# Kernel optimization log

Measured on AMD Instinct MI355X. Metric: run time of the kernel, lower is better.

Reference implementation:

```python
import jax, jax.numpy as jnp
import numpy as np

DIM = 128
HEADS = 4
GH, GW = 14, 14
N = GH * GW            # 196
POS_DIM = (DIM // 4) // 4  # 8, per DynamicPosBias(dim//4): pos_dim = (dim//4)//4
B_ = 1024
NW = 64
EPS = 1e-5


def _make_bias_tables():
    # biases: all relative (dh, dw) offsets, shape ((2*GH-1)*(2*GW-1), 2)
    h = np.arange(1 - GH, GH)
    w = np.arange(1 - GW, GW)
    bh, bw = np.meshgrid(h, w, indexing='ij')
    biases = np.stack([bh.ravel(), bw.ravel()], axis=1).astype(np.float32)
    # relative_position_index: (N, N) int
    ch, cw = np.meshgrid(np.arange(GH), np.arange(GW), indexing='ij')
    coords = np.stack([ch.ravel(), cw.ravel()])          # (2, N)
    rel = coords[:, :, None] - coords[:, None, :]        # (2, N, N)
    rel = rel.transpose(1, 2, 0).copy()
    rel[:, :, 0] += GH - 1
    rel[:, :, 1] += GW - 1
    rel[:, :, 0] *= 2 * GW - 1
    idx = rel.sum(-1).astype(np.int32)                   # (N, N)
    return jnp.asarray(biases), jnp.asarray(idx)


def setup_inputs() -> dict:
    key = jax.random.key(0)
    ks = jax.random.split(key, 12)
    s_in = 1.0 / np.sqrt(DIM)
    s_p = 1.0 / np.sqrt(POS_DIM)
    biases, rel_idx = _make_bias_tables()
    return {
        'x': jax.random.normal(ks[0], (B_, N, DIM), jnp.float32),
        'mask': jnp.zeros((NW, N, N), jnp.float32),
        # qkv / proj (stored as (in, out), i.e. torch weight transposed)
        'qkv_w': jax.random.normal(ks[1], (DIM, 3 * DIM), jnp.float32) * s_in,
        'qkv_b': jnp.zeros((3 * DIM,), jnp.float32),
        'proj_w': jax.random.normal(ks[2], (DIM, DIM), jnp.float32) * s_in,
        'proj_b': jnp.zeros((DIM,), jnp.float32),
        # DynamicPosBias params
        'pos_proj_w': jax.random.normal(ks[3], (2, POS_DIM), jnp.float32) * 0.5,
        'pos_proj_b': jnp.zeros((POS_DIM,), jnp.float32),
        'ln1_w': jnp.ones((POS_DIM,), jnp.float32), 'ln1_b': jnp.zeros((POS_DIM,), jnp.float32),
        'fc1_w': jax.random.normal(ks[4], (POS_DIM, POS_DIM), jnp.float32) * s_p,
        'fc1_b': jnp.zeros((POS_DIM,), jnp.float32),
        'ln2_w': jnp.ones((POS_DIM,), jnp.float32), 'ln2_b': jnp.zeros((POS_DIM,), jnp.float32),
        'fc2_w': jax.random.normal(ks[5], (POS_DIM, POS_DIM), jnp.float32) * s_p,
        'fc2_b': jnp.zeros((POS_DIM,), jnp.float32),
        'ln3_w': jnp.ones((POS_DIM,), jnp.float32), 'ln3_b': jnp.zeros((POS_DIM,), jnp.float32),
        'fc3_w': jax.random.normal(ks[6], (POS_DIM, HEADS), jnp.float32) * s_p,
        'fc3_b': jnp.zeros((HEADS,), jnp.float32),
        'biases': biases,       # ((2GH-1)*(2GW-1), 2) float32
        'rel_idx': rel_idx,     # (N, N) int32
    }


def _ln(x, w, b):
    mu = x.mean(-1, keepdims=True)
    var = ((x - mu) ** 2).mean(-1, keepdims=True)
    return (x - mu) * jax.lax.rsqrt(var + EPS) * w + b


def reference(x, mask, qkv_w, qkv_b, proj_w, proj_b,
              pos_proj_w, pos_proj_b,
              ln1_w, ln1_b, fc1_w, fc1_b,
              ln2_w, ln2_b, fc2_w, fc2_b,
              ln3_w, ln3_b, fc3_w, fc3_b,
              biases, rel_idx):
    B, n, C = x.shape
    hd = C // HEADS
    scale = hd ** -0.5

    qkv = (x @ qkv_w + qkv_b).reshape(B, n, 3, HEADS, hd)
    q, k, v = jnp.moveaxis(qkv, 2, 0)          # each (B, n, H, hd)
    q = q * scale
    attn = jnp.einsum('bqhd,bkhd->bhqk', q, k)  # (B, H, n, n)

    # DynamicPosBias (residual=False): pos3(pos2(pos1(pos_proj(biases))))
    p = biases @ pos_proj_w + pos_proj_b
    p = jax.nn.relu(_ln(p, ln1_w, ln1_b)) @ fc1_w + fc1_b
    p = jax.nn.relu(_ln(p, ln2_w, ln2_b)) @ fc2_w + fc2_b
    p = jax.nn.relu(_ln(p, ln3_w, ln3_b)) @ fc3_w + fc3_b   # (L, H)
    rpb = p[rel_idx]                            # (n, n, H) gather
    attn = attn + jnp.transpose(rpb, (2, 0, 1))[None]

    nW = mask.shape[0]
    attn = attn.reshape(B // nW, nW, HEADS, n, n) + mask[None, :, None]
    attn = jax.nn.softmax(attn.reshape(B, HEADS, n, n), axis=-1)

    out = jnp.einsum('bhqk,bkhd->bqhd', attn, v).reshape(B, n, C)
    return out @ proj_w + proj_b
```

## Files before the change

kernel.cpp:

```cpp
#include <hip/hip_runtime.h>
#include <stdint.h>

#define N_TOK 196
#define DIM   128
#define HEADS 4
#define NWIN  64
#define SCALE 0.17677669529663687f
#define PS_LD 232

typedef __bf16 bf16x8 __attribute__((ext_vector_type(8)));
typedef float  f32x4  __attribute__((ext_vector_type(4)));

__device__ __forceinline__ unsigned short f2bf(float f) {
  unsigned r;
  asm("v_cvt_pk_bf16_f32 %0, %1, %2" : "=v"(r) : "v"(f), "v"(f));
  return (unsigned short)r;
}
__device__ __forceinline__ unsigned pack2(float a, float b) {
  unsigned r;
  asm("v_cvt_pk_bf16_f32 %0, %1, %2" : "=v"(r) : "v"(a), "v"(b));
  return r;
}

__global__ void prep_kernel(
    const float* __restrict__ qkv_w, const float* __restrict__ proj_w,
    const float* __restrict__ biases,
    const float* __restrict__ pos_proj_w, const float* __restrict__ pos_proj_b,
    const float* __restrict__ ln1_w, const float* __restrict__ ln1_b,
    const float* __restrict__ fc1_w, const float* __restrict__ fc1_b,
    const float* __restrict__ ln2_w, const float* __restrict__ ln2_b,
    const float* __restrict__ fc2_w, const float* __restrict__ fc2_b,
    const float* __restrict__ ln3_w, const float* __restrict__ ln3_b,
    const float* __restrict__ fc3_w, const float* __restrict__ fc3_b,
    unsigned short* __restrict__ wqkv_t, unsigned short* __restrict__ wproj_t,
    float* __restrict__ ptab)
{
  const int tid = threadIdx.x, blk = blockIdx.x;
  if (blk < 3) {
    int r = blk * 256 + tid;
    if (r < 729) {
      float v[8], t[8];
      float b0 = biases[2*r], b1 = biases[2*r+1];
      for (int j = 0; j < 8; ++j)
        v[j] = b0 * pos_proj_w[j] + b1 * pos_proj_w[8+j] + pos_proj_b[j];
      const float* lws[3] = {ln1_w, ln2_w, ln3_w};
      const float* lbs[3] = {ln1_b, ln2_b, ln3_b};
      const float* fws[3] = {fc1_w, fc2_w, fc3_w};
      const float* fbs[3] = {fc1_b, fc2_b, fc3_b};
      for (int L = 0; L < 3; ++L) {
        float mu = 0.f;  for (int j=0;j<8;++j) mu += v[j];  mu *= 0.125f;
        float var = 0.f; for (int j=0;j<8;++j){ float d=v[j]-mu; var+=d*d; } var *= 0.125f;
        float rs = rsqrtf(var + 1e-5f);
        for (int j=0;j<8;++j){ float u=(v[j]-mu)*rs*lws[L][j]+lbs[L][j]; t[j]=fmaxf(u,0.f); }
        int nout = (L==2) ? 4 : 8;
        for (int o=0;o<nout;++o){ float s=fbs[L][o]; for (int j=0;j<8;++j) s += t[j]*fws[L][j*nout+o]; v[o]=s; }
      }
      for (int hh=0; hh<4; ++hh) ptab[r*4+hh] = v[hh];
    }
  } else if (blk < 7) {
    for (int i = (blk-3)*256 + tid; i < 384*128; i += 1024) {
      int col = i >> 7, k = i & 127;
      wqkv_t[i] = f2bf(qkv_w[k*384 + col]);
    }
  } else {
    for (int i = tid; i < 128*128; i += 256) {
      int col = i >> 7, k = i & 127;
      wproj_t[i] = f2bf(proj_w[k*128 + col]);
    }
  }
}

__global__ void comb_kernel(const int* __restrict__ rel_idx,
                            const float* __restrict__ ptab,
                            const float* __restrict__ mask,
                            float* __restrict__ combT)
{
  int blk = blockIdx.x;
  int w = blk / 196, k = blk - w*196;
  int q = threadIdx.x;
  if (q < N_TOK) {
    int idx = rel_idx[q*N_TOK + k];
    float mv = mask[((size_t)w*N_TOK + q)*N_TOK + k];
    #pragma unroll
    for (int h = 0; h < 4; ++h)
      combT[((size_t)(w*4 + h)*196 + k)*196 + q] = ptab[idx*4 + h] + mv;
  }
}

__launch_bounds__(256, 2)
__global__ void qkv_kernel(const float* __restrict__ x,
                           const float* __restrict__ qkv_b,
                           const unsigned short* __restrict__ wqkv_t,
                           unsigned short* __restrict__ q_g,
                           unsigned short* __restrict__ k_g,
                           unsigned short* __restrict__ vt_g)
{
  const int tid = threadIdx.x;
  const int wave = tid >> 6, lane = tid & 63, lr = lane & 15, lg = lane >> 4;
  const int b = blockIdx.x;
  const float* xb = x + (size_t)b * (N_TOK*DIM);

  bf16x8 wf[6][4];
  float  bq[6];
  f32x4  bv[6];
  #pragma unroll
  for (int i = 0; i < 6; ++i) {
    const int g = wave*6 + i;
    #pragma unroll
    for (int kc = 0; kc < 4; ++kc)
      wf[i][kc] = *(const bf16x8*)(wqkv_t + (g*16 + lr)*128 + kc*32 + lg*8);
    if (g < 16) {
      bq[i] = qkv_b[g*16 + lr];
      bv[i] = (f32x4){0.f,0.f,0.f,0.f};
    } else {
      bq[i] = 0.f;
      #pragma unroll
      for (int r = 0; r < 4; ++r) bv[i][r] = qkv_b[g*16 + lg*4 + r];
    }
  }

  auto load_xf = [&](int rt, bf16x8* xf) {
    const int arow = rt*16 + lr;
    #pragma unroll
    for (int kc = 0; kc < 4; ++kc) {
      union { unsigned u[4]; bf16x8 v; } c;
      if (arow < N_TOK) {
        float4 p0 = *(const float4*)(xb + arow*DIM + kc*32 + lg*8);
        float4 p1 = *(const float4*)(xb + arow*DIM + kc*32 + lg*8 + 4);
        c.u[0] = pack2(p0.x, p0.y); c.u[1] = pack2(p0.z, p0.w);
        c.u[2] = pack2(p1.x, p1.y); c.u[3] = pack2(p1.z, p1.w);
      } else {
        c.u[0] = c.u[1] = c.u[2] = c.u[3] = 0u;
      }
      xf[kc] = c.v;
    }
  };

  bf16x8 xf[4], xfn[4];
  load_xf(0, xf);
  for (int rt = 0; rt < 13; ++rt) {
    if (rt < 12) load_xf(rt + 1, xfn);
    #pragma unroll
    for (int i = 0; i < 6; ++i) {
      const int g = wave*6 + i;
      f32x4 acc = {0.f,0.f,0.f,0.f};
      if (g >= 16) {
        #pragma unroll
        for (int kc = 0; kc < 4; ++kc)
          acc = __builtin_amdgcn_mfma_f32_16x16x32_bf16(wf[i][kc], xf[kc], acc, 0, 0, 0);
        const int dt = g - 16;
        #pragma unroll
        for (int r = 0; r < 4; ++r)
          vt_g[((size_t)b*128 + dt*16 + lg*4 + r)*224 + rt*16 + lr] =
              f2bf(acc[r] + bv[i][r]);
      } else {
        #pragma unroll
        for (int kc = 0; kc < 4; ++kc)
          acc = __builtin_amdgcn_mfma_f32_16x16x32_bf16(xf[kc], wf[i][kc], acc, 0, 0, 0);
        const int cs = (g < 8) ? g*16 : (g-8)*16;
        unsigned short* dst = (g < 8) ? q_g : k_g;
        const float mul = (g < 8) ? SCALE : 1.f;
        #pragma unroll
        for (int r = 0; r < 4; ++r)
          dst[((size_t)(b*4 + (cs>>5))*208 + rt*16 + lg*4 + r)*32 + (cs&31) + lr] =
              f2bf((acc[r] + bq[i]) * mul);
      }
    }
    #pragma unroll
    for (int kc = 0; kc < 4; ++kc) xf[kc] = xfn[kc];
  }
}

__launch_bounds__(256, 3)
__global__ void attn_kernel(const unsigned short* __restrict__ q_g,
                            const unsigned short* __restrict__ k_g,
                            const unsigned short* __restrict__ vt_g,
                            const float* __restrict__ combT,
                            float* __restrict__ out)
{
  __shared__ unsigned short psw_all[4*16*PS_LD];
  const int tid = threadIdx.x;
  const int wave = tid >> 6, lane = tid & 63, lr = lane & 15, lg = lane >> 4;
  const int wgt = blockIdx.x;
  const int v  = (wgt & 7)*512 + (wgt >> 3);
  const int bi = v & 15, wh = v >> 4;
  const int b  = bi*64 + (wh >> 2), h = wh & 3;
  const int bh = b*4 + h;
  unsigned short* psw = psw_all + wave*(16*PS_LD);

  for (int i = lane; i < 256; i += 64)
    psw[(i >> 4)*PS_LD + 208 + (i & 15)] = 0;

  const unsigned short* qb = q_g + (size_t)bh*(208*32);
  const unsigned short* kb = k_g + (size_t)bh*(208*32);
  const unsigned short* vb = vt_g + (size_t)bh*(32*224);
  const float* cbase = combT + (size_t)wh*(196*196);

  bf16x8 kfr[13];
  #pragma unroll
  for (int kt = 0; kt < 13; ++kt)
    kfr[kt] = *(const bf16x8*)(kb + (kt*16 + lr)*32 + lg*8);

  for (int qt = wave; qt < 13; qt += 4) {
    bf16x8 aq = *(const bf16x8*)(qb + (qt*16 + lr)*32 + lg*8);

    f32x4 s[13];
    #pragma unroll
    for (int kt = 0; kt < 13; ++kt) {
      int c = kt*16 + lr;
      s[kt] = (c < N_TOK) ? *(const f32x4*)(cbase + (size_t)c*196 + qt*16 + lg*4)
                          : (f32x4){0.f,0.f,0.f,0.f};
    }

    __builtin_amdgcn_s_setprio(1);
    #pragma unroll
    for (int kt = 0; kt < 13; ++kt)
      s[kt] = __builtin_amdgcn_mfma_f32_16x16x32_bf16(aq, kfr[kt], s[kt], 0, 0, 0);
    __builtin_amdgcn_s_setprio(0);

    #pragma unroll
    for (int kt = 0; kt < 13; ++kt) {
      #pragma unroll
      for (int r = 0; r < 4; ++r) s[kt][r] = __expf(s[kt][r]);
    }
    if (lr >= 4) s[12] = (f32x4){0.f,0.f,0.f,0.f};

    float linv[4];
    #pragma unroll
    for (int r = 0; r < 4; ++r) {
      float ssum = 0.f;
      #pragma unroll
      for (int kt = 0; kt < 13; ++kt) ssum += s[kt][r];
      #pragma unroll
      for (int off = 1; off < 16; off <<= 1) ssum += __shfl_xor(ssum, off);
      linv[r] = 1.f / ssum;
    }

    #pragma unroll
    for (int r = 0; r < 4; ++r) {
      int prow = lg*4 + r;
      #pragma unroll
      for (int kt = 0; kt < 13; ++kt)
        psw[prow*PS_LD + kt*16 + lr] = f2bf(s[kt][r]);
    }
    asm volatile("s_waitcnt lgkmcnt(0)" ::: "memory");

    __builtin_amdgcn_s_setprio(1);
    #pragma unroll
    for (int c2 = 0; c2 < 2; ++c2) {
      f32x4 o = {0.f,0.f,0.f,0.f};
      #pragma unroll
      for (int kc = 0; kc < 7; ++kc) {
        bf16x8 ap = *(const bf16x8*)(psw + lr*PS_LD + kc*32 + lg*8);
        bf16x8 bv = *(const bf16x8*)(vb + (c2*16 + lr)*224 + kc*32 + lg*8);
        o = __builtin_amdgcn_mfma_f32_16x16x32_bf16(ap, bv, o, 0, 0, 0);
      }
      #pragma unroll
      for (int r = 0; r < 4; ++r) {
        int row = qt*16 + lg*4 + r;
        if (row < N_TOK)
          out[((size_t)b*N_TOK + row)*DIM + h*32 + c2*16 + lr] = o[r] * linv[r];
      }
    }
    __builtin_amdgcn_s_setprio(0);
  }
}

__launch_bounds__(256, 4)
__global__ void proj_kernel(float* __restrict__ out,
                            const unsigned short* __restrict__ wproj_t,
                            const float* __restrict__ proj_b)
{
  __shared__ unsigned short aos[64*136];
  const int tid = threadIdx.x;
  const int wave = tid >> 6, lane = tid & 63, lr = lane & 15, lg = lane >> 4;
  const size_t row0 = (size_t)blockIdx.x * 64;
  const float* src = out + row0*DIM;

  bf16x8 wf[2][4];
  float bias[2];
  #pragma unroll
  for (int i = 0; i < 2; ++i) {
    int ct = wave*2 + i;
    bias[i] = proj_b[ct*16 + lr];
    #pragma unroll
    for (int kc = 0; kc < 4; ++kc)
      wf[i][kc] = *(const bf16x8*)(wproj_t + (ct*16 + lr)*128 + kc*32 + lg*8);
  }

  for (int i = tid; i < 64*32; i += 256) {
    int lrow = i >> 5, c4 = i & 31;
    float4 v = ((const float4*)src)[i];
    ((uint2*)aos)[lrow*34 + c4] = make_uint2(pack2(v.x, v.y), pack2(v.z, v.w));
  }
  __syncthreads();

  for (int rt = 0; rt < 4; ++rt) {
    bf16x8 af[4];
    #pragma unroll
    for (int kc = 0; kc < 4; ++kc)
      af[kc] = *(const bf16x8*)(aos + (rt*16 + lr)*136 + kc*32 + lg*8);
    #pragma unroll
    for (int i = 0; i < 2; ++i) {
      f32x4 acc = {0.f,0.f,0.f,0.f};
      #pragma unroll
      for (int kc = 0; kc < 4; ++kc)
        acc = __builtin_amdgcn_mfma_f32_16x16x32_bf16(af[kc], wf[i][kc], acc, 0, 0, 0);
      #pragma unroll
      for (int r = 0; r < 4; ++r) {
        size_t grow = row0 + rt*16 + lg*4 + r;
        out[grow*DIM + (wave*2 + i)*16 + lr] = acc[r] + bias[i];
      }
    }
  }
}

extern "C" void kernel_launch(void* const* d_in, const int* in_sizes, int n_in,
                              void* d_out, int out_size, void* d_ws, size_t ws_size,
                              hipStream_t stream)
{
  const float* x          = (const float*)d_in[0];
  const float* mask       = (const float*)d_in[1];
  const float* qkv_w      = (const float*)d_in[2];
  const float* qkv_b      = (const float*)d_in[3];
  const float* proj_w     = (const float*)d_in[4];
  const float* proj_b     = (const float*)d_in[5];
  const float* pos_proj_w = (const float*)d_in[6];
  const float* pos_proj_b = (const float*)d_in[7];
  const float* ln1_w = (const float*)d_in[8];
  const float* ln1_b = (const float*)d_in[9];
  const float* fc1_w = (const float*)d_in[10];
  const float* fc1_b = (const float*)d_in[11];
  const float* ln2_w = (const float*)d_in[12];
  const float* ln2_b = (const float*)d_in[13];
  const float* fc2_w = (const float*)d_in[14];
  const float* fc2_b = (const float*)d_in[15];
  const float* ln3_w = (const float*)d_in[16];
  const float* ln3_b = (const float*)d_in[17];
  const float* fc3_w = (const float*)d_in[18];
  const float* fc3_b = (const float*)d_in[19];
  const float* biases = (const float*)d_in[20];
  const int*   rel_idx = (const int*)d_in[21];

  char* ws = (char*)d_ws;
  unsigned short* wqkv_t  = (unsigned short*)(ws);
  unsigned short* wproj_t = (unsigned short*)(ws + 98304);
  float*          ptab    = (float*)(ws + 131072);
  float*          combT   = (float*)(ws + 147456);
  unsigned short* q_g     = (unsigned short*)(ws + 39485696);
  unsigned short* k_g     = (unsigned short*)(ws + 94011648);
  unsigned short* vt_g    = (unsigned short*)(ws + 148537600);
  float* out = (float*)d_out;

  prep_kernel<<<8, 256, 0, stream>>>(qkv_w, proj_w, biases, pos_proj_w, pos_proj_b,
      ln1_w, ln1_b, fc1_w, fc1_b, ln2_w, ln2_b, fc2_w, fc2_b,
      ln3_w, ln3_b, fc3_w, fc3_b, wqkv_t, wproj_t, ptab);
  comb_kernel<<<NWIN*N_TOK, 256, 0, stream>>>(rel_idx, ptab, mask, combT);
  qkv_kernel<<<1024, 256, 0, stream>>>(x, qkv_b, wqkv_t, q_g, k_g, vt_g);
  attn_kernel<<<1024*HEADS, 256, 0, stream>>>(q_g, k_g, vt_g, combT, out);
  proj_kernel<<<(1024*N_TOK)/64, 256, 0, stream>>>(out, wproj_t, proj_b);
}
```

Baseline: 374.4 us.

## Prefetch next bias tile in attention loop and use native exp2

The attention loop is restructured into a lambda body that loads the next query tile's combined bias/mask values while processing the current tile, using double-buffered register arrays. This hides global-load latency behind the MFMA work. The base-2 conversion factor is folded into the Q scale and the combined bias table, so softmax can call the native v_exp_f32 instruction directly. Occupancy is lowered from 3 to 2 blocks per SM to make room for the extra registers, which reduces latency hiding between waves.

```diff
diff --git a/kernel.cpp b/kernel.cpp
--- a/kernel.cpp
+++ b/kernel.cpp
@@ -6,6 +6,7 @@
 #define HEADS 4
 #define NWIN  64
 #define SCALE 0.17677669529663687f
+#define LOG2E 1.4426950408889634f
 #define PS_LD 232
 
 typedef __bf16 bf16x8 __attribute__((ext_vector_type(8)));
@@ -19,6 +20,11 @@
 __device__ __forceinline__ unsigned pack2(float a, float b) {
   unsigned r;
   asm("v_cvt_pk_bf16_f32 %0, %1, %2" : "=v"(r) : "v"(a), "v"(b));
+  return r;
+}
+__device__ __forceinline__ float fexp2(float x) {
+  float r;
+  asm("v_exp_f32 %0, %1" : "=v"(r) : "v"(x));
   return r;
 }
 
@@ -83,7 +89,7 @@
     float mv = mask[((size_t)w*N_TOK + q)*N_TOK + k];
     #pragma unroll
     for (int h = 0; h < 4; ++h)
-      combT[((size_t)(w*4 + h)*196 + k)*196 + q] = ptab[idx*4 + h] + mv;
+      combT[((size_t)(w*4 + h)*196 + k)*196 + q] = (ptab[idx*4 + h] + mv) * LOG2E;
   }
 }
 
@@ -159,7 +165,7 @@
           acc = __builtin_amdgcn_mfma_f32_16x16x32_bf16(xf[kc], wf[i][kc], acc, 0, 0, 0);
         const int cs = (g < 8) ? g*16 : (g-8)*16;
         unsigned short* dst = (g < 8) ? q_g : k_g;
-        const float mul = (g < 8) ? SCALE : 1.f;
+        const float mul = (g < 8) ? (SCALE * LOG2E) : 1.f;
         #pragma unroll
         for (int r = 0; r < 4; ++r)
           dst[((size_t)(b*4 + (cs>>5))*208 + rt*16 + lg*4 + r)*32 + (cs&31) + lr] =
@@ -171,7 +177,7 @@
   }
 }
 
-__launch_bounds__(256, 3)
+__launch_bounds__(256, 2)
 __global__ void attn_kernel(const unsigned short* __restrict__ q_g,
                             const unsigned short* __restrict__ k_g,
                             const unsigned short* __restrict__ vt_g,
@@ -201,16 +207,18 @@
   for (int kt = 0; kt < 13; ++kt)
     kfr[kt] = *(const bf16x8*)(kb + (kt*16 + lr)*32 + lg*8);
 
-  for (int qt = wave; qt < 13; qt += 4) {
-    bf16x8 aq = *(const bf16x8*)(qb + (qt*16 + lr)*32 + lg*8);
-
-    f32x4 s[13];
+  auto load_cmb = [&](int qt, f32x4* s) {
     #pragma unroll
     for (int kt = 0; kt < 13; ++kt) {
       int c = kt*16 + lr;
       s[kt] = (c < N_TOK) ? *(const f32x4*)(cbase + (size_t)c*196 + qt*16 + lg*4)
                           : (f32x4){0.f,0.f,0.f,0.f};
     }
+  };
+
+  auto body = [&](int qt, f32x4* s, int qtn, f32x4* sn) {
+    if (qtn < 13) load_cmb(qtn, sn);
+    bf16x8 aq = *(const bf16x8*)(qb + (qt*16 + lr)*32 + lg*8);
 
     __builtin_amdgcn_s_setprio(1);
     #pragma unroll
@@ -221,7 +229,7 @@
     #pragma unroll
     for (int kt = 0; kt < 13; ++kt) {
       #pragma unroll
-      for (int r = 0; r < 4; ++r) s[kt][r] = __expf(s[kt][r]);
+      for (int r = 0; r < 4; ++r) s[kt][r] = fexp2(s[kt][r]);
     }
     if (lr >= 4) s[12] = (f32x4){0.f,0.f,0.f,0.f};
 
@@ -263,6 +271,19 @@
       }
     }
     __builtin_amdgcn_s_setprio(0);
+  };
+
+  f32x4 sA[13], sB[13];
+  load_cmb(wave, sA);
+  if (wave == 0) {
+    body(0, sA, 4, sB);
+    body(4, sB, 8, sA);
+    body(8, sA, 12, sB);
+    body(12, sB, 99, sA);
+  } else {
+    body(wave, sA, wave + 4, sB);
+    body(wave + 4, sB, wave + 8, sA);
+    body(wave + 8, sA, 99, sB);
   }
 }
 
```

Result: slower. 386.1 us (+3.1%).
